# Kernel tuning notes

Measured on AMD Instinct MI355X. Metric: run time of the kernel, lower is better.

The kernel has to match this reference:

```python
import jax, jax.numpy as jnp
import numpy as np

TEMPERATURE = 0.5
EPS = 1e-8
NEG = -1e30  # effectively -inf for masked logits


def _l2norm(x):
    n = jnp.sqrt(jnp.sum(x * x, axis=1, keepdims=True))
    return x / jnp.maximum(n, EPS)


def setup_inputs() -> dict:
    key = jax.random.key(0)
    ks = jax.random.split(key, 4)
    N, D = 2048, 128
    return {f"projection_image_aug{i+1}": jax.random.normal(ks[i], (N, D), dtype=jnp.float32)
            for i in range(4)}


def reference(projection_image_aug1, projection_image_aug2,
              projection_image_aug3, projection_image_aug4):
    zs = [projection_image_aug1.astype(jnp.float32),
          projection_image_aug2.astype(jnp.float32),
          projection_image_aug3.astype(jnp.float32),
          projection_image_aug4.astype(jnp.float32)]
    N = zs[0].shape[0]
    k = len(zs)
    z = jnp.concatenate(zs[:2], axis=0)        # [2N, D]
    z_all = jnp.concatenate(zs, axis=0)        # [kN, D]
    # cosine sim via normalize + matmul (same math as broadcast CosineSimilarity)
    sim = _l2norm(z) @ _l2norm(z_all).T / TEMPERATURE   # [2N, kN]

    rows = jnp.arange(2 * N)
    half = rows // N                 # 0 for first N rows, 1 for second
    idx = rows % N
    cols = jnp.arange(k * N)
    block = cols // N
    # mask: diagonal entries of every N-block except the target block (1-half)
    diag = (cols[None, :] % N) == idx[:, None]
    mask = diag & (block[None, :] != (1 - half)[:, None])
    sim_m = jnp.where(mask, NEG, sim)
    # positive column: aug2 partner for rows<N, aug1 partner for rows>=N
    target_col = (1 - half) * N + idx
    pos = jnp.take_along_axis(sim_m, target_col[:, None], axis=1)[:, 0]
    # cross_entropy(reduction='sum') / (2N)
    loss = jnp.sum(jax.nn.logsumexp(sim_m, axis=1) - pos) / (2 * N)
    return loss
```

## Files before the change

kernel.cpp:

```cpp
#include <hip/hip_runtime.h>
#include <hip/hip_bf16.h>


#define NN      2048
#define DD      128
#define TWO_N   4096
#define FOUR_N  8192
#define BM      128
#define BN      128
#define GT      8
#define CTG     8

using frag_ab = __attribute__((ext_vector_type(8))) short;
using f32x4   = __attribute__((ext_vector_type(4))) float;

__device__ inline void gl_lds16(const short* g, short* l) {
  __builtin_amdgcn_global_load_lds(
      (const __attribute__((address_space(1))) void*)g,
      (__attribute__((address_space(3))) void*)l, 16, 0, 0);
}

__device__ inline int swz(int chunk) {
  return (chunk & ~15) | ((chunk & 15) ^ ((chunk >> 4) & 15));
}

__global__ __launch_bounds__(256) void knorm(const float* __restrict__ p0,
                                             const float* __restrict__ p1,
                                             const float* __restrict__ p2,
                                             const float* __restrict__ p3,
                                             short* __restrict__ Bn,
                                             float* __restrict__ out) {
  if (blockIdx.x == 0 && threadIdx.x == 0) out[0] = 0.0f;
  int wave = threadIdx.x >> 6, lane = threadIdx.x & 63;
  int row = blockIdx.x * 4 + wave;
  int q = row >> 11, idx = row & (NN - 1);
  const float* src = (q == 0) ? p0 : (q == 1) ? p1 : (q == 2) ? p2 : p3;
  const float2* s2 = (const float2*)(src + (size_t)idx * DD);
  float2 v = s2[lane];
  float ss = v.x * v.x + v.y * v.y;
  #pragma unroll
  for (int sh = 1; sh < 64; sh <<= 1) ss += __shfl_xor(ss, sh, 64);
  float inv = 1.0f / fmaxf(sqrtf(ss), 1e-8f);
  __hip_bfloat162 o;
  o.x = __float2bfloat16(v.x * inv);
  o.y = __float2bfloat16(v.y * inv);
  ((__hip_bfloat162*)(Bn + (size_t)row * DD))[lane] = o;
}

__global__ __launch_bounds__(1024, 4) void kgemm(const short* __restrict__ Bn,
                                                 float* __restrict__ pS) {
  __shared__ short sA[BM * DD];
  __shared__ short sB[2][BN * DD];
  __shared__ float sS[BM][4];

  int t = threadIdx.x, wave = t >> 6, lane = t & 63;
  int quad = lane >> 4, l16 = lane & 15;
  int rowQ = wave >> 2, colQ = wave & 3;

  const short* gA = Bn + (size_t)blockIdx.x * BM * DD;
  const short* gB0 = Bn + (size_t)blockIdx.y * (GT * BN) * DD;

  #pragma unroll
  for (int i = 0; i < 2; ++i) {
    int c0 = i * 1024 + wave * 64;
    gl_lds16(gA + (size_t)swz(c0 + lane) * 8, sA + (size_t)c0 * 8);
    gl_lds16(gB0 + (size_t)swz(c0 + lane) * 8, sB[0] + (size_t)c0 * 8);
  }
  __syncthreads();

  frag_ab a[4][2];
  #pragma unroll
  for (int k = 0; k < 4; ++k)
    #pragma unroll
    for (int rf = 0; rf < 2; ++rf) {
      int r_ = rowQ * 32 + rf * 16 + l16;
      a[k][rf] = *(const frag_ab*)&sA[(size_t)((r_ << 4) | ((k * 4 + quad) ^ l16)) * 8];
    }

  float sAcc[2][4];
  #pragma unroll
  for (int rf = 0; rf < 2; ++rf)
    #pragma unroll
    for (int r = 0; r < 4; ++r) sAcc[rf][r] = 0.f;

  #pragma unroll 1
  for (int g = 0; g < GT; ++g) {
    if (g < GT - 1) {
      const short* gBn = gB0 + (size_t)(g + 1) * BN * DD;
      short* dst = sB[(g + 1) & 1];
      #pragma unroll
      for (int i = 0; i < 2; ++i) {
        int c0 = i * 1024 + wave * 64;
        gl_lds16(gBn + (size_t)swz(c0 + lane) * 8, dst + (size_t)c0 * 8);
      }
    }
    const short* sBg = sB[g & 1];

    f32x4 acc[2][2];
    #pragma unroll
    for (int rf = 0; rf < 2; ++rf)
      #pragma unroll
      for (int cf = 0; cf < 2; ++cf) acc[rf][cf] = (f32x4){0.f, 0.f, 0.f, 0.f};

    #pragma unroll
    for (int k = 0; k < 4; ++k) {
      frag_ab b[2];
      #pragma unroll
      for (int cf = 0; cf < 2; ++cf) {
        int r_ = colQ * 32 + cf * 16 + l16;
        b[cf] = *(const frag_ab*)&sBg[(size_t)((r_ << 4) | ((k * 4 + quad) ^ l16)) * 8];
      }
      #pragma unroll
      for (int rf = 0; rf < 2; ++rf)
        #pragma unroll
        for (int cf = 0; cf < 2; ++cf)
          acc[rf][cf] = __builtin_amdgcn_mfma_f32_16x16x32_bf16(a[k][rf], b[cf], acc[rf][cf], 0, 0, 0);
    }

    #pragma unroll
    for (int rf = 0; rf < 2; ++rf)
      #pragma unroll
      for (int r = 0; r < 4; ++r) {
        #pragma unroll
        for (int cf = 0; cf < 2; ++cf)
          sAcc[rf][r] += __expf(fmaf(acc[rf][cf][r], 2.0f, -2.0f));
      }
    __syncthreads();
  }

  #pragma unroll
  for (int rf = 0; rf < 2; ++rf)
    #pragma unroll
    for (int r = 0; r < 4; ++r) {
      float s = sAcc[rf][r];
      #pragma unroll
      for (int sh = 1; sh < 16; sh <<= 1) s += __shfl_xor(s, sh, 64);
      if (l16 == 0) sS[rowQ * 32 + rf * 16 + quad * 4 + r][colQ] = s;
    }
  __syncthreads();
  if (t < BM)
    pS[(size_t)(blockIdx.x * BM + t) * CTG + blockIdx.y] =
        (sS[t][0] + sS[t][1]) + (sS[t][2] + sS[t][3]);
}

__global__ __launch_bounds__(256) void kfin(const short* __restrict__ Bn,
                                            const float* __restrict__ pS,
                                            float* __restrict__ out) {
  int t = threadIdx.x, wave = t >> 6, lane = t & 63;
  int grBase = blockIdx.x * BM;
  __shared__ float sRed[4];

  float wloss = 0.f;
  for (int rr = wave; rr < BM; rr += 4) {
    int gr = grBase + rr;
    int idx = gr & (NN - 1), half = gr >> 11;
    float S = (lane < CTG) ? pS[(size_t)gr * CTG + lane] : 0.f;
    #pragma unroll
    for (int sh = 1; sh < 8; sh <<= 1) S += __shfl_xor(S, sh, 64);
    unsigned int ua = ((const unsigned int*)(Bn + (size_t)gr * DD))[lane];
    unsigned int ub = ((const unsigned int*)(Bn + (size_t)((1 - half) * NN + idx) * DD))[lane];
    unsigned int uc = ((const unsigned int*)(Bn + (size_t)(2 * NN + idx) * DD))[lane];
    unsigned int ud = ((const unsigned int*)(Bn + (size_t)(3 * NN + idx) * DD))[lane];
    float a0 = __uint_as_float((ua & 0xffffu) << 16), a1 = __uint_as_float(ua & 0xffff0000u);
    float b0 = __uint_as_float((ub & 0xffffu) << 16), b1 = __uint_as_float(ub & 0xffff0000u);
    float c0 = __uint_as_float((uc & 0xffffu) << 16), c1 = __uint_as_float(uc & 0xffff0000u);
    float d0 = __uint_as_float((ud & 0xffffu) << 16), d1 = __uint_as_float(ud & 0xffff0000u);
    float daa = a0 * a0 + a1 * a1;
    float dab = a0 * b0 + a1 * b1;
    float dac = a0 * c0 + a1 * c1;
    float dad = a0 * d0 + a1 * d1;
    #pragma unroll
    for (int sh = 1; sh < 64; sh <<= 1) {
      daa += __shfl_xor(daa, sh, 64);
      dab += __shfl_xor(dab, sh, 64);
      dac += __shfl_xor(dac, sh, 64);
      dad += __shfl_xor(dad, sh, 64);
    }
    float Sc = S - __expf(fmaf(daa, 2.0f, -2.0f))
                 - __expf(fmaf(dac, 2.0f, -2.0f))
                 - __expf(fmaf(dad, 2.0f, -2.0f));
    float loss = (2.0f + __logf(Sc)) - 2.0f * dab;
    if (lane == 0) wloss += loss;
  }
  if (lane == 0) sRed[wave] = wloss;
  __syncthreads();
  if (t == 0)
    atomicAdd(out, (sRed[0] + sRed[1] + sRed[2] + sRed[3]) * (1.0f / (float)TWO_N));
}

extern "C" void kernel_launch(void* const* d_in, const int* in_sizes, int n_in,
                              void* d_out, int out_size, void* d_ws, size_t ws_size,
                              hipStream_t stream) {
  (void)in_sizes; (void)n_in; (void)out_size; (void)ws_size;
  const float* p0 = (const float*)d_in[0];
  const float* p1 = (const float*)d_in[1];
  const float* p2 = (const float*)d_in[2];
  const float* p3 = (const float*)d_in[3];

  short* Bn = (short*)d_ws;
  float* pS = (float*)((char*)d_ws + (size_t)FOUR_N * DD * sizeof(short));
  float* out = (float*)d_out;

  knorm<<<FOUR_N / 4, 256, 0, stream>>>(p0, p1, p2, p3, Bn, out);
  kgemm<<<dim3(TWO_N / BM, CTG), 1024, 0, stream>>>(Bn, pS);
  kfin<<<TWO_N / BM, 256, 0, stream>>>(Bn, pS, out);
}
```

Baseline: 102.4 us.

## Drop LDS staging in GEMM, load fragments directly from global with smaller tiles

The GEMM kernel no longer stages A and B tiles in shared memory with async global-to-LDS copies and barriers. Each wave now loads its A fragments (64 rows) and B fragments (16 columns per wave) straight from global/L2 into registers, and the tile shape changes to 64x1024 per 512-thread block. The exponent uses exp2 with a folded constant. The final kernel also uses more, smaller blocks. This removes the LDS traffic and per-iteration barriers and raises the block count, at the cost of more redundant global/L2 reads and less data reuse.

```diff
diff --git a/kernel.cpp b/kernel.cpp
--- a/kernel.cpp
+++ b/kernel.cpp
@@ -6,23 +6,11 @@
 #define DD      128
 #define TWO_N   4096
 #define FOUR_N  8192
-#define BM      128
-#define BN      128
-#define GT      8
 #define CTG     8
+#define C2L2E   2.8853900817779268f
 
 using frag_ab = __attribute__((ext_vector_type(8))) short;
 using f32x4   = __attribute__((ext_vector_type(4))) float;
-
-__device__ inline void gl_lds16(const short* g, short* l) {
-  __builtin_amdgcn_global_load_lds(
-      (const __attribute__((address_space(1))) void*)g,
-      (__attribute__((address_space(3))) void*)l, 16, 0, 0);
-}
-
-__device__ inline int swz(int chunk) {
-  return (chunk & ~15) | ((chunk & 15) ^ ((chunk >> 4) & 15));
-}
 
 __global__ __launch_bounds__(256) void knorm(const float* __restrict__ p0,
                                              const float* __restrict__ p1,
@@ -47,111 +35,84 @@
   ((__hip_bfloat162*)(Bn + (size_t)row * DD))[lane] = o;
 }
 
-__global__ __launch_bounds__(1024, 4) void kgemm(const short* __restrict__ Bn,
-                                                 float* __restrict__ pS) {
-  __shared__ short sA[BM * DD];
-  __shared__ short sB[2][BN * DD];
-  __shared__ float sS[BM][4];
+__global__ __launch_bounds__(512, 4) void kgemm(const short* __restrict__ Bn,
+                                                float* __restrict__ pS) {
+  __shared__ float sS[64][CTG + 1];
 
   int t = threadIdx.x, wave = t >> 6, lane = t & 63;
   int quad = lane >> 4, l16 = lane & 15;
-  int rowQ = wave >> 2, colQ = wave & 3;
+  int bx = blockIdx.x, by = blockIdx.y;
 
-  const short* gA = Bn + (size_t)blockIdx.x * BM * DD;
-  const short* gB0 = Bn + (size_t)blockIdx.y * (GT * BN) * DD;
+  const short* gA = Bn + (size_t)(bx * 64 + l16) * DD + quad * 8;
+  frag_ab a[4][4];
+  #pragma unroll
+  for (int rf = 0; rf < 4; ++rf)
+    #pragma unroll
+    for (int k = 0; k < 4; ++k)
+      a[k][rf] = *(const frag_ab*)(gA + (size_t)rf * 16 * DD + k * 32);
 
+  const short* gB = Bn + (size_t)(by * 1024 + wave * 16 + l16) * DD + quad * 8;
+
+  float sAcc[4][4];
   #pragma unroll
-  for (int i = 0; i < 2; ++i) {
-    int c0 = i * 1024 + wave * 64;
-    gl_lds16(gA + (size_t)swz(c0 + lane) * 8, sA + (size_t)c0 * 8);
-    gl_lds16(gB0 + (size_t)swz(c0 + lane) * 8, sB[0] + (size_t)c0 * 8);
-  }
-  __syncthreads();
-
-  frag_ab a[4][2];
-  #pragma unroll
-  for (int k = 0; k < 4; ++k)
-    #pragma unroll
-    for (int rf = 0; rf < 2; ++rf) {
-      int r_ = rowQ * 32 + rf * 16 + l16;
-      a[k][rf] = *(const frag_ab*)&sA[(size_t)((r_ << 4) | ((k * 4 + quad) ^ l16)) * 8];
-    }
-
-  float sAcc[2][4];
-  #pragma unroll
-  for (int rf = 0; rf < 2; ++rf)
+  for (int rf = 0; rf < 4; ++rf)
     #pragma unroll
     for (int r = 0; r < 4; ++r) sAcc[rf][r] = 0.f;
 
   #pragma unroll 1
-  for (int g = 0; g < GT; ++g) {
-    if (g < GT - 1) {
-      const short* gBn = gB0 + (size_t)(g + 1) * BN * DD;
-      short* dst = sB[(g + 1) & 1];
+  for (int g = 0; g < 8; ++g) {
+    const short* gBg = gB + (size_t)g * 128 * DD;
+    frag_ab bb[4];
+    #pragma unroll
+    for (int k = 0; k < 4; ++k)
+      bb[k] = *(const frag_ab*)(gBg + k * 32);
+
+    f32x4 acc[4];
+    #pragma unroll
+    for (int rf = 0; rf < 4; ++rf) acc[rf] = (f32x4){0.f, 0.f, 0.f, 0.f};
+    #pragma unroll
+    for (int k = 0; k < 4; ++k)
       #pragma unroll
-      for (int i = 0; i < 2; ++i) {
-        int c0 = i * 1024 + wave * 64;
-        gl_lds16(gBn + (size_t)swz(c0 + lane) * 8, dst + (size_t)c0 * 8);
-      }
-    }
-    const short* sBg = sB[g & 1];
-
-    f32x4 acc[2][2];
-    #pragma unroll
-    for (int rf = 0; rf < 2; ++rf)
-      #pragma unroll
-      for (int cf = 0; cf < 2; ++cf) acc[rf][cf] = (f32x4){0.f, 0.f, 0.f, 0.f};
+      for (int rf = 0; rf < 4; ++rf)
+        acc[rf] = __builtin_amdgcn_mfma_f32_16x16x32_bf16(a[k][rf], bb[k], acc[rf], 0, 0, 0);
 
     #pragma unroll
-    for (int k = 0; k < 4; ++k) {
-      frag_ab b[2];
+    for (int rf = 0; rf < 4; ++rf)
       #pragma unroll
-      for (int cf = 0; cf < 2; ++cf) {
-        int r_ = colQ * 32 + cf * 16 + l16;
-        b[cf] = *(const frag_ab*)&sBg[(size_t)((r_ << 4) | ((k * 4 + quad) ^ l16)) * 8];
-      }
-      #pragma unroll
-      for (int rf = 0; rf < 2; ++rf)
-        #pragma unroll
-        for (int cf = 0; cf < 2; ++cf)
-          acc[rf][cf] = __builtin_amdgcn_mfma_f32_16x16x32_bf16(a[k][rf], b[cf], acc[rf][cf], 0, 0, 0);
-    }
-
-    #pragma unroll
-    for (int rf = 0; rf < 2; ++rf)
-      #pragma unroll
-      for (int r = 0; r < 4; ++r) {
-        #pragma unroll
-        for (int cf = 0; cf < 2; ++cf)
-          sAcc[rf][r] += __expf(fmaf(acc[rf][cf][r], 2.0f, -2.0f));
-      }
-    __syncthreads();
+      for (int r = 0; r < 4; ++r)
+        sAcc[rf][r] += __builtin_amdgcn_exp2f(fmaf(acc[rf][r], C2L2E, -C2L2E));
   }
 
   #pragma unroll
-  for (int rf = 0; rf < 2; ++rf)
+  for (int rf = 0; rf < 4; ++rf)
     #pragma unroll
     for (int r = 0; r < 4; ++r) {
       float s = sAcc[rf][r];
-      #pragma unroll
-      for (int sh = 1; sh < 16; sh <<= 1) s += __shfl_xor(s, sh, 64);
-      if (l16 == 0) sS[rowQ * 32 + rf * 16 + quad * 4 + r][colQ] = s;
+      s += __shfl_xor(s, 1, 64);
+      s += __shfl_xor(s, 2, 64);
+      s += __shfl_xor(s, 4, 64);
+      s += __shfl_xor(s, 8, 64);
+      if (l16 == 0) sS[rf * 16 + quad * 4 + r][wave] = s;
     }
   __syncthreads();
-  if (t < BM)
-    pS[(size_t)(blockIdx.x * BM + t) * CTG + blockIdx.y] =
-        (sS[t][0] + sS[t][1]) + (sS[t][2] + sS[t][3]);
+  if (t < 64) {
+    const float* row = sS[t];
+    pS[(size_t)(bx * 64 + t) * CTG + by] =
+        ((row[0] + row[1]) + (row[2] + row[3])) +
+        ((row[4] + row[5]) + (row[6] + row[7]));
+  }
 }
 
 __global__ __launch_bounds__(256) void kfin(const short* __restrict__ Bn,
                                             const float* __restrict__ pS,
                                             float* __restrict__ out) {
   int t = threadIdx.x, wave = t >> 6, lane = t & 63;
-  int grBase = blockIdx.x * BM;
+  int grBase = blockIdx.x * 16;
   __shared__ float sRed[4];
 
   float wloss = 0.f;
-  for (int rr = wave; rr < BM; rr += 4) {
+  #pragma unroll 1
+  for (int rr = wave; rr < 16; rr += 4) {
     int gr = grBase + rr;
     int idx = gr & (NN - 1), half = gr >> 11;
     float S = (lane < CTG) ? pS[(size_t)gr * CTG + lane] : 0.f;
@@ -202,6 +163,6 @@
   float* out = (float*)d_out;
 
   knorm<<<FOUR_N / 4, 256, 0, stream>>>(p0, p1, p2, p3, Bn, out);
-  kgemm<<<dim3(TWO_N / BM, CTG), 1024, 0, stream>>>(Bn, pS);
-  kfin<<<TWO_N / BM, 256, 0, stream>>>(Bn, pS, out);
+  kgemm<<<dim3(TWO_N / 64, CTG), 512, 0, stream>>>(Bn, pS);
+  kfin<<<TWO_N / 16, 256, 0, stream>>>(Bn, pS, out);
 }
```

Result: faster. 95.94 us (-6.3%).
